# Optimization experiments

Measured on AMD Instinct MI355X. Metric: run time of the kernel, lower is better.

## Reference

```python
import jax, jax.numpy as jnp
import numpy as np

N_NODES = 50000
N_EDGES = 800000
IN_CH = 128
HID_CH = 128
OUT_CH = 10
NUM_GRAPHS = 128


def setup_inputs() -> dict:
    key = jax.random.key(0)
    ks = jax.random.split(key, 10)
    x = jax.random.normal(ks[0], (N_NODES, IN_CH), dtype=jnp.float32)
    edge_index = jax.random.randint(ks[1], (2, N_EDGES), 0, N_NODES, dtype=jnp.int64)
    batch = jnp.sort(jax.random.randint(ks[2], (N_NODES,), 0, NUM_GRAPHS, dtype=jnp.int64))
    s1 = 1.0 / np.sqrt(IN_CH)
    s2 = 1.0 / np.sqrt(HID_CH)
    W1 = jax.random.uniform(ks[3], (IN_CH, HID_CH), jnp.float32, -s1, s1)
    b1 = jnp.zeros((HID_CH,), jnp.float32)
    W2 = jax.random.uniform(ks[4], (HID_CH, HID_CH), jnp.float32, -s2, s2)
    b2 = jnp.zeros((HID_CH,), jnp.float32)
    Wc = jax.random.uniform(ks[5], (HID_CH, OUT_CH), jnp.float32, -s2, s2)
    bc = jax.random.uniform(ks[6], (OUT_CH,), jnp.float32, -s2, s2)
    return {"x": x, "edge_index": edge_index, "batch": batch,
            "W1": W1, "b1": b1, "W2": W2, "b2": b2, "Wc": Wc, "bc": bc}


def _gcn_norm(edge_index, num_nodes):
    # add self-loops, compute symmetric normalization deg^-1/2[src]*deg^-1/2[dst]
    loop = jnp.arange(num_nodes, dtype=edge_index.dtype)
    src = jnp.concatenate([edge_index[0], loop])
    dst = jnp.concatenate([edge_index[1], loop])
    deg = jax.ops.segment_sum(jnp.ones_like(dst, dtype=jnp.float32), dst,
                              num_segments=num_nodes)
    dinv = jnp.where(deg > 0, jax.lax.rsqrt(deg), 0.0)
    norm = dinv[src] * dinv[dst]
    return src, dst, norm


def _gcn_conv(h, src, dst, norm, W, b, num_nodes):
    h = h @ W                                    # [N, out]
    msg = h[src] * norm[:, None]                 # [E+N, out] gather + scale
    agg = jax.ops.segment_sum(msg, dst, num_segments=num_nodes)
    return agg + b


def reference(x, edge_index, batch, W1, b1, W2, b2, Wc, bc):
    n = x.shape[0]
    src, dst, norm = _gcn_norm(edge_index, n)
    h = jax.nn.relu(_gcn_conv(x, src, dst, norm, W1, b1, n))
    h = jax.nn.relu(_gcn_conv(h, src, dst, norm, W2, b2, n))
    # global mean pool over graphs
    sums = jax.ops.segment_sum(h, batch, num_segments=NUM_GRAPHS)
    cnts = jax.ops.segment_sum(jnp.ones((n,), jnp.float32), batch,
                               num_segments=NUM_GRAPHS)
    pooled = sums / jnp.maximum(cnts, 1.0)[:, None]
    # dropout is identity in eval mode
    return pooled @ Wc + bc
```

## Files before the change

kernel.cpp:

```cpp
#include <hip/hip_runtime.h>

#define N_NODES 50000
#define N_EDGES 800000
#define CH 128
#define NOUT 10
#define NUM_GRAPHS 128
#define GR 64
#define GEMM_BLOCKS ((N_NODES + GR - 1) / GR)
#define FILL_SEGS 200
#define FILL_CHUNK (N_EDGES / FILL_SEGS)
#define DST_RANGE (N_NODES / 8)
#define DEG_CAP 64

typedef __attribute__((ext_vector_type(8))) short bf16x8;
typedef __attribute__((ext_vector_type(4))) float f32x4;

union FragU { uint4 u; bf16x8 s; };

__device__ __forceinline__ unsigned pack_bf16(float a, float b) {
    unsigned ua = __float_as_uint(a), ub = __float_as_uint(b);
    ua += 0x7fffu + ((ua >> 16) & 1u);
    ub += 0x7fffu + ((ub >> 16) & 1u);
    return (ua >> 16) | (ub & 0xffff0000u);
}

__device__ __forceinline__ unsigned short cvt_bf16(float v) {
    unsigned u = __float_as_uint(v);
    u += 0x7fffu + ((u >> 16) & 1u);
    return (unsigned short)(u >> 16);
}

__global__ __launch_bounds__(256) void k_prep(const float* __restrict__ W1,
                                              const float* __restrict__ W2,
                                              unsigned short* __restrict__ Wb1,
                                              unsigned short* __restrict__ Wb2,
                                              int* __restrict__ fill_pos,
                                              float* __restrict__ psum) {
    if (blockIdx.x < 2) {
        const float* W = blockIdx.x ? W2 : W1;
        unsigned short* Wb = blockIdx.x ? Wb2 : Wb1;
        for (int i = threadIdx.x; i < CH * CH; i += 256) {
            int k = i >> 7, n = i & 127;
            Wb[((((k >> 3) << 7) + n) << 3) + (k & 7)] = cvt_bf16(W[i]);
        }
    } else if (blockIdx.x < 198) {
        int idx = (blockIdx.x - 2) * 256 + threadIdx.x;
        if (idx < N_NODES) fill_pos[idx] = 0;
    } else {
        psum[(blockIdx.x - 198) * 256 + threadIdx.x] = 0.f;
    }
}

template <bool SCALE>
__device__ __forceinline__ void gemm_body9(const float* __restrict__ X,
                                           const unsigned short* __restrict__ Wb,
                                           unsigned short* __restrict__ Yb,
                                           const int* __restrict__ cnt,
                                           int bid) {
    const int tid = threadIdx.x;
    const int w = tid >> 6;
    const int lane = tid & 63;
    const int m = lane & 15;
    const int quad = lane >> 4;
    const int row0 = bid * GR + w * 16;

    int row_a = row0 + m;
    if (row_a > N_NODES - 1) row_a = N_NODES - 1;
    const float4* Xr = (const float4*)(X + (size_t)row_a * CH) + quad * 2;

    float4 a[8];
    #pragma unroll
    for (int ks = 0; ks < 4; ++ks) {
        a[ks * 2]     = Xr[ks * 8];
        a[ks * 2 + 1] = Xr[ks * 8 + 1];
    }

    f32x4 acc[8];
    #pragma unroll
    for (int ct = 0; ct < 8; ++ct) acc[ct] = (f32x4){0.f, 0.f, 0.f, 0.f};

    const uint4* Wq = (const uint4*)Wb;
    #pragma unroll
    for (int ks = 0; ks < 4; ++ks) {
        FragU af;
        af.u.x = pack_bf16(a[ks * 2].x, a[ks * 2].y);
        af.u.y = pack_bf16(a[ks * 2].z, a[ks * 2].w);
        af.u.z = pack_bf16(a[ks * 2 + 1].x, a[ks * 2 + 1].y);
        af.u.w = pack_bf16(a[ks * 2 + 1].z, a[ks * 2 + 1].w);
        const int kg = ks * 4 + quad;
        #pragma unroll
        for (int ct = 0; ct < 8; ++ct) {
            FragU bfu;
            bfu.u = Wq[kg * 128 + ct * 16 + m];
            acc[ct] = __builtin_amdgcn_mfma_f32_16x16x32_bf16(af.s, bfu.s, acc[ct], 0, 0, 0);
        }
    }

    #pragma unroll
    for (int r = 0; r < 4; ++r) {
        int row = row0 + quad * 4 + r;
        if (row < N_NODES) {
            float dv = SCALE ? rsqrtf((float)(cnt[row] + 1)) : 1.0f;
            unsigned short* yrow = Yb + (size_t)row * CH + m;
            #pragma unroll
            for (int ct = 0; ct < 8; ++ct)
                yrow[ct * 16] = cvt_bf16(SCALE ? acc[ct][r] * dv : acc[ct][r]);
        }
    }
}

__global__ __launch_bounds__(256) void k_gemm_fill(const float* __restrict__ X,
                                                   const unsigned short* __restrict__ Wb,
                                                   unsigned short* __restrict__ Yb,
                                                   const int* __restrict__ src,
                                                   const int* __restrict__ dst,
                                                   int* __restrict__ fill_pos,
                                                   int* __restrict__ csr_src) {
    if (blockIdx.x < GEMM_BLOCKS) {
        gemm_body9<false>(X, Wb, Yb, nullptr, blockIdx.x);
    } else {
        const int b = blockIdx.x - GEMM_BLOCKS;
        const int rng = b & 7;
        const int seg = b >> 3;
        const int lo = rng * DST_RANGE, hi = lo + DST_RANGE;
        const int base = seg * FILL_CHUNK;
        for (int it = threadIdx.x * 4; it < FILL_CHUNK; it += 1024) {
            int e = base + it;
            int4 d4 = *(const int4*)(dst + e);
            #pragma unroll
            for (int k = 0; k < 4; ++k) {
                int d = (&d4.x)[k];
                if (d >= lo && d < hi) {
                    int slot = atomicAdd(&fill_pos[d], 1);
                    if (slot < DEG_CAP) csr_src[(d << 6) + slot] = src[e + k];
                }
            }
        }
    }
}

__global__ __launch_bounds__(256) void k_gemm9b(const float* __restrict__ X,
                                                const unsigned short* __restrict__ Wb,
                                                unsigned short* __restrict__ Yb,
                                                const int* __restrict__ cnt) {
    gemm_body9<true>(X, Wb, Yb, cnt, blockIdx.x);
}

template <bool HAS_W, bool POOL>
__device__ __forceinline__ void gather_body(const unsigned* __restrict__ tb,
                                            const int* __restrict__ csr_src,
                                            const int* __restrict__ cnt,
                                            const float* __restrict__ bias,
                                            float* __restrict__ h,
                                            const int* __restrict__ batch,
                                            float* __restrict__ psum) {
    const int wid = threadIdx.x >> 6;
    const int lane = threadIdx.x & 63;
    const int sub = lane >> 4;
    const int cidx = lane & 15;
    const int v = blockIdx.x * 4 + wid;

    int lenc = cnt[v];
    const float dv = rsqrtf((float)(lenc + 1));
    int len = lenc > DEG_CAP ? DEG_CAP : lenc;

    int u_l = 0;
    float w_l = 0.f;
    if (lane < len) {
        u_l = csr_src[(v << 6) + lane];
        if (HAS_W) w_l = rsqrtf((float)(cnt[u_l] + 1));
    }

    const uint4* tbq = (const uint4*)tb;
    float x[8];
    #pragma unroll
    for (int t = 0; t < 8; ++t) x[t] = 0.f;

    int j = 0;
    for (; j + 8 <= len; j += 8) {
        int i0 = j + sub, i1 = j + 4 + sub;
        int ua = __shfl(u_l, i0);
        int ub = __shfl(u_l, i1);
        float wa = HAS_W ? __shfl(w_l, i0) : 1.f;
        float wb = HAS_W ? __shfl(w_l, i1) : 1.f;
        uint4 qa = tbq[(size_t)ua * 16 + cidx];
        uint4 qb = tbq[(size_t)ub * 16 + cidx];
        #pragma unroll
        for (int t = 0; t < 4; ++t) {
            unsigned ra = ((const unsigned*)&qa)[t];
            x[2 * t]     = fmaf(wa, __uint_as_float(ra << 16), x[2 * t]);
            x[2 * t + 1] = fmaf(wa, __uint_as_float(ra & 0xffff0000u), x[2 * t + 1]);
        }
        #pragma unroll
        for (int t = 0; t < 4; ++t) {
            unsigned rb = ((const unsigned*)&qb)[t];
            x[2 * t]     = fmaf(wb, __uint_as_float(rb << 16), x[2 * t]);
            x[2 * t + 1] = fmaf(wb, __uint_as_float(rb & 0xffff0000u), x[2 * t + 1]);
        }
    }
    for (; j < len; j += 4) {
        int idx = j + sub;
        bool act = idx < len;
        int idx_c = act ? idx : 0;
        int u = __shfl(u_l, idx_c);
        float w;
        if (HAS_W) { float ws = __shfl(w_l, idx_c); w = act ? ws : 0.f; }
        else       { w = act ? 1.f : 0.f; }
        uint4 q = tbq[(size_t)u * 16 + cidx];
        #pragma unroll
        for (int t = 0; t < 4; ++t) {
            unsigned r = ((const unsigned*)&q)[t];
            x[2 * t]     = fmaf(w, __uint_as_float(r << 16), x[2 * t]);
            x[2 * t + 1] = fmaf(w, __uint_as_float(r & 0xffff0000u), x[2 * t + 1]);
        }
    }
    {
        uint4 q = tbq[(size_t)v * 16 + cidx];
        float w = (sub == 0) ? (HAS_W ? dv : 1.f) : 0.f;
        #pragma unroll
        for (int t = 0; t < 4; ++t) {
            unsigned r = ((const unsigned*)&q)[t];
            x[2 * t]     = fmaf(w, __uint_as_float(r << 16), x[2 * t]);
            x[2 * t + 1] = fmaf(w, __uint_as_float(r & 0xffff0000u), x[2 * t + 1]);
        }
    }

    #pragma unroll
    for (int t = 0; t < 8; ++t) {
        x[t] += __shfl_xor(x[t], 16);
        x[t] += __shfl_xor(x[t], 32);
    }

    const float4* b4 = (const float4*)bias;
    float4 b0 = b4[cidx * 2], b1 = b4[cidx * 2 + 1];
    float4 o0, o1;
    o0.x = fmaxf(fmaf(dv, x[0], b0.x), 0.f);
    o0.y = fmaxf(fmaf(dv, x[1], b0.y), 0.f);
    o0.z = fmaxf(fmaf(dv, x[2], b0.z), 0.f);
    o0.w = fmaxf(fmaf(dv, x[3], b0.w), 0.f);
    o1.x = fmaxf(fmaf(dv, x[4], b1.x), 0.f);
    o1.y = fmaxf(fmaf(dv, x[5], b1.y), 0.f);
    o1.z = fmaxf(fmaf(dv, x[6], b1.z), 0.f);
    o1.w = fmaxf(fmaf(dv, x[7], b1.w), 0.f);

    if (POOL) {
        __shared__ float sh[4][128];
        __shared__ int sg[4];
        if (lane == 0) sg[wid] = batch[v];
        if (sub == 0) {
            *(float4*)&sh[wid][cidx * 8]     = o0;
            *(float4*)&sh[wid][cidx * 8 + 4] = o1;
        }
        __syncthreads();
        const int tid = threadIdx.x;
        if (tid < 128) {
            int g0 = sg[0], g1 = sg[1], g2 = sg[2], g3 = sg[3];
            float v0 = sh[0][tid], v1 = sh[1][tid], v2 = sh[2][tid], v3 = sh[3][tid];
            if (g0 == g3) {
                atomicAdd(&psum[g0 * CH + tid], v0 + v1 + v2 + v3);
            } else {
                if (g0 == g1) v1 += v0; else atomicAdd(&psum[g0 * CH + tid], v0);
                if (g1 == g2) v2 += v1; else atomicAdd(&psum[g1 * CH + tid], v1);
                if (g2 == g3) v3 += v2; else atomicAdd(&psum[g2 * CH + tid], v2);
                atomicAdd(&psum[g3 * CH + tid], v3);
            }
        }
    } else {
        if (sub == 0) {
            float4* hq = (float4*)(h + (size_t)v * CH);
            hq[cidx * 2]     = o0;
            hq[cidx * 2 + 1] = o1;
        }
    }
}

__global__ __launch_bounds__(256) void k_gather_hw(const unsigned* __restrict__ tb,
                                                   const int* __restrict__ csr_src,
                                                   const int* __restrict__ cnt,
                                                   const float* __restrict__ b,
                                                   float* __restrict__ h) {
    gather_body<true, false>(tb, csr_src, cnt, b, h, nullptr, nullptr);
}

__global__ __launch_bounds__(256) void k_gather_pool(const unsigned* __restrict__ tb,
                                                     const int* __restrict__ csr_src,
                                                     const int* __restrict__ cnt,
                                                     const float* __restrict__ b,
                                                     const int* __restrict__ batch,
                                                     float* __restrict__ psum) {
    gather_body<false, true>(tb, csr_src, cnt, b, nullptr, batch, psum);
}

__global__ __launch_bounds__(128) void k_classify(const float* __restrict__ psum,
                                                  const int* __restrict__ batch,
                                                  const float* __restrict__ Wc,
                                                  const float* __restrict__ bc,
                                                  float* __restrict__ out) {
    __shared__ float p[CH];
    __shared__ float sinv;
    int g = blockIdx.x;
    int tid = threadIdx.x;
    if (tid == 0) {
        int lo = 0, hi = N_NODES;
        while (lo < hi) { int mid = (lo + hi) >> 1; if (batch[mid] < g) lo = mid + 1; else hi = mid; }
        int start = lo;
        lo = 0; hi = N_NODES;
        while (lo < hi) { int mid = (lo + hi) >> 1; if (batch[mid] < g + 1) lo = mid + 1; else hi = mid; }
        sinv = 1.0f / fmaxf((float)(lo - start), 1.0f);
    }
    __syncthreads();
    p[tid] = psum[g * CH + tid] * sinv;
    __syncthreads();
    if (tid < NOUT) {
        float acc = bc[tid];
        #pragma unroll 4
        for (int k = 0; k < CH; ++k) acc += p[k] * Wc[k * NOUT + tid];
        out[g * NOUT + tid] = acc;
    }
}

extern "C" void kernel_launch(void* const* d_in, const int* in_sizes, int n_in,
                              void* d_out, int out_size, void* d_ws, size_t ws_size,
                              hipStream_t stream) {
    const float* x     = (const float*)d_in[0];
    const int*   ei    = (const int*)d_in[1];
    const int*   batch = (const int*)d_in[2];
    const float* W1    = (const float*)d_in[3];
    const float* b1    = (const float*)d_in[4];
    const float* W2    = (const float*)d_in[5];
    const float* b2    = (const float*)d_in[6];
    const float* Wc    = (const float*)d_in[7];
    const float* bc    = (const float*)d_in[8];
    float* out = (float*)d_out;

    const int* src = ei;
    const int* dst = ei + N_EDGES;

    int*            fill_pos = (int*)d_ws;
    int*            csr_src  = fill_pos + N_NODES;
    unsigned short* wb1      = (unsigned short*)(csr_src + (size_t)N_NODES * DEG_CAP);
    unsigned short* wb2      = wb1 + CH * CH;
    unsigned short* tb       = wb2 + CH * CH;
    float*          hbuf     = (float*)(tb + (size_t)N_NODES * CH);
    float*          psum     = hbuf + (size_t)N_NODES * CH;

    k_prep<<<198 + 64, 256, 0, stream>>>(W1, W2, wb1, wb2, fill_pos, psum);

    k_gemm_fill<<<GEMM_BLOCKS + FILL_SEGS * 8, 256, 0, stream>>>(
        x, wb1, tb, src, dst, fill_pos, csr_src);

    k_gather_hw<<<N_NODES / 4, 256, 0, stream>>>((unsigned*)tb, csr_src, fill_pos, b1, hbuf);

    k_gemm9b<<<GEMM_BLOCKS, 256, 0, stream>>>(hbuf, wb2, tb, fill_pos);

    k_gather_pool<<<N_NODES / 4, 256, 0, stream>>>((unsigned*)tb, csr_src, fill_pos, b2,
                                                   batch, psum);

    k_classify<<<NUM_GRAPHS, 128, 0, stream>>>(psum, batch, Wc, bc, out);
}
```

Baseline: 246.5 us.

## Store hidden layer in bf16, vectorize GEMM output stores, unroll gather loop

The first gather now writes the hidden activations as packed bf16 instead of fp32. The second GEMM loads these bf16 A-fragments directly, with no fp32 load-and-convert step. The GEMM B-fragment indexing is permuted so each lane owns 8 contiguous output columns, which lets the output be written as a single 16-byte store instead of eight scalar 2-byte stores. The CSR fill loads src as an int4 vector, its blocks are ordered before the GEMM blocks, and the gather loop is restructured to issue up to four row loads before accumulating. The aim is less memory traffic and more loads in flight, at the cost of extra bf16 rounding on the intermediate activations.

```diff
diff --git a/kernel.cpp b/kernel.cpp
--- a/kernel.cpp
+++ b/kernel.cpp
@@ -9,6 +9,7 @@
 #define GEMM_BLOCKS ((N_NODES + GR - 1) / GR)
 #define FILL_SEGS 200
 #define FILL_CHUNK (N_EDGES / FILL_SEGS)
+#define FILL_BLOCKS (FILL_SEGS * 8)
 #define DST_RANGE (N_NODES / 8)
 #define DEG_CAP 64
 
@@ -51,8 +52,8 @@
     }
 }
 
-template <bool SCALE>
-__device__ __forceinline__ void gemm_body9(const float* __restrict__ X,
+template <bool SCALE, bool ABF16>
+__device__ __forceinline__ void gemm_body9(const void* __restrict__ X,
                                            const unsigned short* __restrict__ Wb,
                                            unsigned short* __restrict__ Yb,
                                            const int* __restrict__ cnt,
@@ -66,33 +67,42 @@
 
     int row_a = row0 + m;
     if (row_a > N_NODES - 1) row_a = N_NODES - 1;
-    const float4* Xr = (const float4*)(X + (size_t)row_a * CH) + quad * 2;
-
-    float4 a[8];
+
+    FragU af[4];
+    if (ABF16) {
+        const uint4* Xr = (const uint4*)((const unsigned short*)X + (size_t)row_a * CH);
+        #pragma unroll
+        for (int ks = 0; ks < 4; ++ks) af[ks].u = Xr[ks * 4 + quad];
+    } else {
+        const float4* Xr = (const float4*)((const float*)X + (size_t)row_a * CH) + quad * 2;
+        float4 a[8];
+        #pragma unroll
+        for (int ks = 0; ks < 4; ++ks) {
+            a[ks * 2]     = Xr[ks * 8];
+            a[ks * 2 + 1] = Xr[ks * 8 + 1];
+        }
+        #pragma unroll
+        for (int ks = 0; ks < 4; ++ks) {
+            af[ks].u.x = pack_bf16(a[ks * 2].x, a[ks * 2].y);
+            af[ks].u.y = pack_bf16(a[ks * 2].z, a[ks * 2].w);
+            af[ks].u.z = pack_bf16(a[ks * 2 + 1].x, a[ks * 2 + 1].y);
+            af[ks].u.w = pack_bf16(a[ks * 2 + 1].z, a[ks * 2 + 1].w);
+        }
+    }
+
+    f32x4 acc[8];
+    #pragma unroll
+    for (int ct = 0; ct < 8; ++ct) acc[ct] = (f32x4){0.f, 0.f, 0.f, 0.f};
+
+    const uint4* Wq = (const uint4*)Wb;
     #pragma unroll
     for (int ks = 0; ks < 4; ++ks) {
-        a[ks * 2]     = Xr[ks * 8];
-        a[ks * 2 + 1] = Xr[ks * 8 + 1];
-    }
-
-    f32x4 acc[8];
-    #pragma unroll
-    for (int ct = 0; ct < 8; ++ct) acc[ct] = (f32x4){0.f, 0.f, 0.f, 0.f};
-
-    const uint4* Wq = (const uint4*)Wb;
-    #pragma unroll
-    for (int ks = 0; ks < 4; ++ks) {
-        FragU af;
-        af.u.x = pack_bf16(a[ks * 2].x, a[ks * 2].y);
-        af.u.y = pack_bf16(a[ks * 2].z, a[ks * 2].w);
-        af.u.z = pack_bf16(a[ks * 2 + 1].x, a[ks * 2 + 1].y);
-        af.u.w = pack_bf16(a[ks * 2 + 1].z, a[ks * 2 + 1].w);
         const int kg = ks * 4 + quad;
         #pragma unroll
         for (int ct = 0; ct < 8; ++ct) {
             FragU bfu;
-            bfu.u = Wq[kg * 128 + ct * 16 + m];
-            acc[ct] = __builtin_amdgcn_mfma_f32_16x16x32_bf16(af.s, bfu.s, acc[ct], 0, 0, 0);
+            bfu.u = Wq[kg * 128 + m * 8 + ct];
+            acc[ct] = __builtin_amdgcn_mfma_f32_16x16x32_bf16(af[ks].s, bfu.s, acc[ct], 0, 0, 0);
         }
     }
 
@@ -100,11 +110,13 @@
     for (int r = 0; r < 4; ++r) {
         int row = row0 + quad * 4 + r;
         if (row < N_NODES) {
-            float dv = SCALE ? rsqrtf((float)(cnt[row] + 1)) : 1.0f;
-            unsigned short* yrow = Yb + (size_t)row * CH + m;
-            #pragma unroll
-            for (int ct = 0; ct < 8; ++ct)
-                yrow[ct * 16] = cvt_bf16(SCALE ? acc[ct][r] * dv : acc[ct][r]);
+            float s = SCALE ? rsqrtf((float)(cnt[row] + 1)) : 1.0f;
+            uint4 o;
+            o.x = pack_bf16(acc[0][r] * s, acc[1][r] * s);
+            o.y = pack_bf16(acc[2][r] * s, acc[3][r] * s);
+            o.z = pack_bf16(acc[4][r] * s, acc[5][r] * s);
+            o.w = pack_bf16(acc[6][r] * s, acc[7][r] * s);
+            *(uint4*)(Yb + (size_t)row * CH + m * 8) = o;
         }
     }
 }
@@ -116,10 +128,8 @@
                                                    const int* __restrict__ dst,
                                                    int* __restrict__ fill_pos,
                                                    int* __restrict__ csr_src) {
-    if (blockIdx.x < GEMM_BLOCKS) {
-        gemm_body9<false>(X, Wb, Yb, nullptr, blockIdx.x);
-    } else {
-        const int b = blockIdx.x - GEMM_BLOCKS;
+    if (blockIdx.x < FILL_BLOCKS) {
+        const int b = blockIdx.x;
         const int rng = b & 7;
         const int seg = b >> 3;
         const int lo = rng * DST_RANGE, hi = lo + DST_RANGE;
@@ -127,23 +137,35 @@
         for (int it = threadIdx.x * 4; it < FILL_CHUNK; it += 1024) {
             int e = base + it;
             int4 d4 = *(const int4*)(dst + e);
+            int4 s4 = *(const int4*)(src + e);
             #pragma unroll
             for (int k = 0; k < 4; ++k) {
                 int d = (&d4.x)[k];
                 if (d >= lo && d < hi) {
                     int slot = atomicAdd(&fill_pos[d], 1);
-                    if (slot < DEG_CAP) csr_src[(d << 6) + slot] = src[e + k];
+                    if (slot < DEG_CAP) csr_src[(d << 6) + slot] = (&s4.x)[k];
                 }
             }
         }
-    }
-}
-
-__global__ __launch_bounds__(256) void k_gemm9b(const float* __restrict__ X,
+    } else {
+        gemm_body9<false, false>(X, Wb, Yb, nullptr, blockIdx.x - FILL_BLOCKS);
+    }
+}
+
+__global__ __launch_bounds__(256) void k_gemm9b(const unsigned short* __restrict__ Xb,
                                                 const unsigned short* __restrict__ Wb,
                                                 unsigned short* __restrict__ Yb,
                                                 const int* __restrict__ cnt) {
-    gemm_body9<true>(X, Wb, Yb, cnt, blockIdx.x);
+    gemm_body9<true, true>(Xb, Wb, Yb, cnt, blockIdx.x);
+}
+
+__device__ __forceinline__ void acc_row(float (&x)[8], uint4 q, float w) {
+    #pragma unroll
+    for (int t = 0; t < 4; ++t) {
+        unsigned r = ((const unsigned*)&q)[t];
+        x[2 * t]     = fmaf(w, __uint_as_float(r << 16), x[2 * t]);
+        x[2 * t + 1] = fmaf(w, __uint_as_float(r & 0xffff0000u), x[2 * t + 1]);
+    }
 }
 
 template <bool HAS_W, bool POOL>
@@ -151,7 +173,7 @@
                                             const int* __restrict__ csr_src,
                                             const int* __restrict__ cnt,
                                             const float* __restrict__ bias,
-                                            float* __restrict__ h,
+                                            unsigned short* __restrict__ hb,
                                             const int* __restrict__ batch,
                                             float* __restrict__ psum) {
     const int wid = threadIdx.x >> 6;
@@ -176,53 +198,44 @@
     #pragma unroll
     for (int t = 0; t < 8; ++t) x[t] = 0.f;
 
-    int j = 0;
-    for (; j + 8 <= len; j += 8) {
-        int i0 = j + sub, i1 = j + 4 + sub;
-        int ua = __shfl(u_l, i0);
-        int ub = __shfl(u_l, i1);
-        float wa = HAS_W ? __shfl(w_l, i0) : 1.f;
-        float wb = HAS_W ? __shfl(w_l, i1) : 1.f;
-        uint4 qa = tbq[(size_t)ua * 16 + cidx];
-        uint4 qb = tbq[(size_t)ub * 16 + cidx];
-        #pragma unroll
-        for (int t = 0; t < 4; ++t) {
-            unsigned ra = ((const unsigned*)&qa)[t];
-            x[2 * t]     = fmaf(wa, __uint_as_float(ra << 16), x[2 * t]);
-            x[2 * t + 1] = fmaf(wa, __uint_as_float(ra & 0xffff0000u), x[2 * t + 1]);
-        }
-        #pragma unroll
-        for (int t = 0; t < 4; ++t) {
-            unsigned rb = ((const unsigned*)&qb)[t];
-            x[2 * t]     = fmaf(wb, __uint_as_float(rb << 16), x[2 * t]);
-            x[2 * t + 1] = fmaf(wb, __uint_as_float(rb & 0xffff0000u), x[2 * t + 1]);
-        }
-    }
-    for (; j < len; j += 4) {
-        int idx = j + sub;
-        bool act = idx < len;
-        int idx_c = act ? idx : 0;
-        int u = __shfl(u_l, idx_c);
-        float w;
-        if (HAS_W) { float ws = __shfl(w_l, idx_c); w = act ? ws : 0.f; }
-        else       { w = act ? 1.f : 0.f; }
-        uint4 q = tbq[(size_t)u * 16 + cidx];
-        #pragma unroll
-        for (int t = 0; t < 4; ++t) {
-            unsigned r = ((const unsigned*)&q)[t];
-            x[2 * t]     = fmaf(w, __uint_as_float(r << 16), x[2 * t]);
-            x[2 * t + 1] = fmaf(w, __uint_as_float(r & 0xffff0000u), x[2 * t + 1]);
-        }
+    const int ng = (len + 3) >> 2;
+    for (int g = 0; g < ng; g += 4) {
+        uint4 q0, q1, q2, q3;
+        float w0, w1, w2, w3;
+        bool h1 = g + 1 < ng, h2 = g + 2 < ng, h3 = g + 3 < ng;
+        {
+            int idx = g * 4 + sub; bool act = idx < len; int ic = act ? idx : 0;
+            int u = __shfl(u_l, ic);
+            w0 = act ? (HAS_W ? __shfl(w_l, ic) : 1.f) : 0.f;
+            q0 = tbq[(size_t)u * 16 + cidx];
+        }
+        if (h1) {
+            int idx = (g + 1) * 4 + sub; bool act = idx < len; int ic = act ? idx : 0;
+            int u = __shfl(u_l, ic);
+            w1 = act ? (HAS_W ? __shfl(w_l, ic) : 1.f) : 0.f;
+            q1 = tbq[(size_t)u * 16 + cidx];
+        }
+        if (h2) {
+            int idx = (g + 2) * 4 + sub; bool act = idx < len; int ic = act ? idx : 0;
+            int u = __shfl(u_l, ic);
+            w2 = act ? (HAS_W ? __shfl(w_l, ic) : 1.f) : 0.f;
+            q2 = tbq[(size_t)u * 16 + cidx];
+        }
+        if (h3) {
+            int idx = (g + 3) * 4 + sub; bool act = idx < len; int ic = act ? idx : 0;
+            int u = __shfl(u_l, ic);
+            w3 = act ? (HAS_W ? __shfl(w_l, ic) : 1.f) : 0.f;
+            q3 = tbq[(size_t)u * 16 + cidx];
+        }
+        acc_row(x, q0, w0);
+        if (h1) acc_row(x, q1, w1);
+        if (h2) acc_row(x, q2, w2);
+        if (h3) acc_row(x, q3, w3);
     }
     {
         uint4 q = tbq[(size_t)v * 16 + cidx];
         float w = (sub == 0) ? (HAS_W ? dv : 1.f) : 0.f;
-        #pragma unroll
-        for (int t = 0; t < 4; ++t) {
-            unsigned r = ((const unsigned*)&q)[t];
-            x[2 * t]     = fmaf(w, __uint_as_float(r << 16), x[2 * t]);
-            x[2 * t + 1] = fmaf(w, __uint_as_float(r & 0xffff0000u), x[2 * t + 1]);
-        }
+        acc_row(x, q, w);
     }
 
     #pragma unroll
@@ -233,23 +246,24 @@
 
     const float4* b4 = (const float4*)bias;
     float4 b0 = b4[cidx * 2], b1 = b4[cidx * 2 + 1];
-    float4 o0, o1;
-    o0.x = fmaxf(fmaf(dv, x[0], b0.x), 0.f);
-    o0.y = fmaxf(fmaf(dv, x[1], b0.y), 0.f);
-    o0.z = fmaxf(fmaf(dv, x[2], b0.z), 0.f);
-    o0.w = fmaxf(fmaf(dv, x[3], b0.w), 0.f);
-    o1.x = fmaxf(fmaf(dv, x[4], b1.x), 0.f);
-    o1.y = fmaxf(fmaf(dv, x[5], b1.y), 0.f);
-    o1.z = fmaxf(fmaf(dv, x[6], b1.z), 0.f);
-    o1.w = fmaxf(fmaf(dv, x[7], b1.w), 0.f);
+    float o[8];
+    o[0] = fmaxf(fmaf(dv, x[0], b0.x), 0.f);
+    o[1] = fmaxf(fmaf(dv, x[1], b0.y), 0.f);
+    o[2] = fmaxf(fmaf(dv, x[2], b0.z), 0.f);
+    o[3] = fmaxf(fmaf(dv, x[3], b0.w), 0.f);
+    o[4] = fmaxf(fmaf(dv, x[4], b1.x), 0.f);
+    o[5] = fmaxf(fmaf(dv, x[5], b1.y), 0.f);
+    o[6] = fmaxf(fmaf(dv, x[6], b1.z), 0.f);
+    o[7] = fmaxf(fmaf(dv, x[7], b1.w), 0.f);
 
     if (POOL) {
         __shared__ float sh[4][128];
         __shared__ int sg[4];
         if (lane == 0) sg[wid] = batch[v];
         if (sub == 0) {
-            *(float4*)&sh[wid][cidx * 8]     = o0;
-            *(float4*)&sh[wid][cidx * 8 + 4] = o1;
+            float4* shp = (float4*)&sh[wid][cidx * 8];
+            shp[0] = (float4){o[0], o[1], o[2], o[3]};
+            shp[1] = (float4){o[4], o[5], o[6], o[7]};
         }
         __syncthreads();
         const int tid = threadIdx.x;
@@ -267,9 +281,12 @@
         }
     } else {
         if (sub == 0) {
-            float4* hq = (float4*)(h + (size_t)v * CH);
-            hq[cidx * 2]     = o0;
-            hq[cidx * 2 + 1] = o1;
+            uint4 ob;
+            ob.x = pack_bf16(o[0], o[1]);
+            ob.y = pack_bf16(o[2], o[3]);
+            ob.z = pack_bf16(o[4], o[5]);
+            ob.w = pack_bf16(o[6], o[7]);
+            *(uint4*)(hb + (size_t)v * CH + cidx * 8) = ob;
         }
     }
 }
@@ -278,8 +295,8 @@
                                                    const int* __restrict__ csr_src,
                                                    const int* __restrict__ cnt,
                                                    const float* __restrict__ b,
-                                                   float* __restrict__ h) {
-    gather_body<true, false>(tb, csr_src, cnt, b, h, nullptr, nullptr);
+                                                   unsigned short* __restrict__ hb) {
+    gather_body<true, false>(tb, csr_src, cnt, b, hb, nullptr, nullptr);
 }
 
 __global__ __launch_bounds__(256) void k_gather_pool(const unsigned* __restrict__ tb,
@@ -341,17 +358,17 @@
     unsigned short* wb1      = (unsigned short*)(csr_src + (size_t)N_NODES * DEG_CAP);
     unsigned short* wb2      = wb1 + CH * CH;
     unsigned short* tb       = wb2 + CH * CH;
-    float*          hbuf     = (float*)(tb + (size_t)N_NODES * CH);
-    float*          psum     = hbuf + (size_t)N_NODES * CH;
+    unsigned short* hb16     = tb + (size_t)N_NODES * CH;
+    float*          psum     = (float*)(hb16 + (size_t)N_NODES * CH);
 
     k_prep<<<198 + 64, 256, 0, stream>>>(W1, W2, wb1, wb2, fill_pos, psum);
 
-    k_gemm_fill<<<GEMM_BLOCKS + FILL_SEGS * 8, 256, 0, stream>>>(
+    k_gemm_fill<<<FILL_BLOCKS + GEMM_BLOCKS, 256, 0, stream>>>(
         x, wb1, tb, src, dst, fill_pos, csr_src);
 
-    k_gather_hw<<<N_NODES / 4, 256, 0, stream>>>((unsigned*)tb, csr_src, fill_pos, b1, hbuf);
-
-    k_gemm9b<<<GEMM_BLOCKS, 256, 0, stream>>>(hbuf, wb2, tb, fill_pos);
+    k_gather_hw<<<N_NODES / 4, 256, 0, stream>>>((unsigned*)tb, csr_src, fill_pos, b1, hb16);
+
+    k_gemm9b<<<GEMM_BLOCKS, 256, 0, stream>>>(hb16, wb2, tb, fill_pos);
 
     k_gather_pool<<<N_NODES / 4, 256, 0, stream>>>((unsigned*)tb, csr_src, fill_pos, b2,
                                                    batch, psum);
```

New measurement: 260.7 us. +5.7%, slower.

## Replace range-partitioned CSR fill with single-pass edge-chunked fill

Applied to the files above, without the earlier changes.

The CSR fill no longer has each edge segment scanned by 8 blocks, each of which keeps only destinations in its own node range. Each block now handles a 2048-edge chunk once, reading dst and src with vector int4 loads and issuing atomics for every edge. This removes the 8x redundant reads of dst and the scalar src loads. In exchange it loses the locality of the atomics and scattered writes within a node range, which may raise cache contention on fill_pos and csr_src.

```diff
diff --git a/kernel.cpp b/kernel.cpp
--- a/kernel.cpp
+++ b/kernel.cpp
@@ -7,9 +7,8 @@
 #define NUM_GRAPHS 128
 #define GR 64
 #define GEMM_BLOCKS ((N_NODES + GR - 1) / GR)
-#define FILL_SEGS 200
-#define FILL_CHUNK (N_EDGES / FILL_SEGS)
-#define DST_RANGE (N_NODES / 8)
+#define FILL_EPB 2048
+#define FILL_BLOCKS ((N_EDGES + FILL_EPB - 1) / FILL_EPB)
 #define DEG_CAP 64
 
 typedef __attribute__((ext_vector_type(8))) short bf16x8;
@@ -120,19 +119,25 @@
         gemm_body9<false>(X, Wb, Yb, nullptr, blockIdx.x);
     } else {
         const int b = blockIdx.x - GEMM_BLOCKS;
-        const int rng = b & 7;
-        const int seg = b >> 3;
-        const int lo = rng * DST_RANGE, hi = lo + DST_RANGE;
-        const int base = seg * FILL_CHUNK;
-        for (int it = threadIdx.x * 4; it < FILL_CHUNK; it += 1024) {
-            int e = base + it;
-            int4 d4 = *(const int4*)(dst + e);
-            #pragma unroll
-            for (int k = 0; k < 4; ++k) {
-                int d = (&d4.x)[k];
-                if (d >= lo && d < hi) {
+        const int base = b * FILL_EPB;
+        int4 d4[2], s4[2];
+        #pragma unroll
+        for (int i = 0; i < 2; ++i) {
+            int e = base + ((int)threadIdx.x + i * 256) * 4;
+            if (e < N_EDGES) {
+                d4[i] = *(const int4*)(dst + e);
+                s4[i] = *(const int4*)(src + e);
+            }
+        }
+        #pragma unroll
+        for (int i = 0; i < 2; ++i) {
+            int e = base + ((int)threadIdx.x + i * 256) * 4;
+            if (e < N_EDGES) {
+                #pragma unroll
+                for (int k = 0; k < 4; ++k) {
+                    int d = (&d4[i].x)[k];
                     int slot = atomicAdd(&fill_pos[d], 1);
-                    if (slot < DEG_CAP) csr_src[(d << 6) + slot] = src[e + k];
+                    if (slot < DEG_CAP) csr_src[(d << 6) + slot] = (&s4[i].x)[k];
                 }
             }
         }
@@ -346,7 +351,7 @@
 
     k_prep<<<198 + 64, 256, 0, stream>>>(W1, W2, wb1, wb2, fill_pos, psum);
 
-    k_gemm_fill<<<GEMM_BLOCKS + FILL_SEGS * 8, 256, 0, stream>>>(
+    k_gemm_fill<<<GEMM_BLOCKS + FILL_BLOCKS, 256, 0, stream>>>(
         x, wb1, tb, src, dst, fill_pos, csr_src);
 
     k_gather_hw<<<N_NODES / 4, 256, 0, stream>>>((unsigned*)tb, csr_src, fill_pos, b1, hbuf);
```

Result: slower. 257.0 us (+4.2%).

## Split gather kernels by channel half and prefetch all neighbor rows upfront

Applied to the files above, without the earlier changes.

Each node's 128-channel aggregation is now split across two blocks, one per 64-channel half. Each wave processes 8 neighbor rows at once (8 lanes per row) instead of 4. All neighbor-row loads, up to 8 per lane, are issued before any accumulation, to raise memory-level parallelism in the latency-bound gather. In exchange there are twice as many blocks, cnt and csr_src are read twice per node, there are more shuffle reductions, and extra registers are held for the prefetched rows.

```diff
diff --git a/kernel.cpp b/kernel.cpp
--- a/kernel.cpp
+++ b/kernel.cpp
@@ -5,12 +5,14 @@
 #define CH 128
 #define NOUT 10
 #define NUM_GRAPHS 128
+#define POOL_CHUNK 50
 #define GR 64
 #define GEMM_BLOCKS ((N_NODES + GR - 1) / GR)
 #define FILL_SEGS 200
 #define FILL_CHUNK (N_EDGES / FILL_SEGS)
 #define DST_RANGE (N_NODES / 8)
 #define DEG_CAP 64
+#define GATHER_BLOCKS (N_NODES / 4 * 2)
 
 typedef __attribute__((ext_vector_type(8))) short bf16x8;
 typedef __attribute__((ext_vector_type(4))) float f32x4;
@@ -146,19 +148,32 @@
     gemm_body9<true>(X, Wb, Yb, cnt, blockIdx.x);
 }
 
+__device__ __forceinline__ void acc_row(float (&x)[8], uint4 q, float w) {
+    #pragma unroll
+    for (int t = 0; t < 4; ++t) {
+        unsigned r = ((const unsigned*)&q)[t];
+        x[2 * t]     = fmaf(w, __uint_as_float(r << 16), x[2 * t]);
+        x[2 * t + 1] = fmaf(w, __uint_as_float(r & 0xffff0000u), x[2 * t + 1]);
+    }
+}
+
 template <bool HAS_W, bool POOL>
-__device__ __forceinline__ void gather_body(const unsigned* __restrict__ tb,
-                                            const int* __restrict__ csr_src,
-                                            const int* __restrict__ cnt,
-                                            const float* __restrict__ bias,
-                                            float* __restrict__ h,
-                                            const int* __restrict__ batch,
-                                            float* __restrict__ psum) {
-    const int wid = threadIdx.x >> 6;
-    const int lane = threadIdx.x & 63;
-    const int sub = lane >> 4;
-    const int cidx = lane & 15;
-    const int v = blockIdx.x * 4 + wid;
+__device__ __forceinline__ void gather_half_body(const uint4* __restrict__ tbq,
+                                                 const int* __restrict__ csr_src,
+                                                 const int* __restrict__ cnt,
+                                                 const float* __restrict__ bias,
+                                                 float* __restrict__ h,
+                                                 const int* __restrict__ batch,
+                                                 float* __restrict__ psum) {
+    const int tid = threadIdx.x;
+    const int wid = tid >> 6;
+    const int lane = tid & 63;
+    const int sub = lane >> 3;
+    const int cidx = lane & 7;
+    const int r = blockIdx.x & 7;
+    const int half = r >> 2;
+    const int vg = (blockIdx.x >> 3) * 4 + (r & 3);
+    const int v = vg * 4 + wid;
 
     int lenc = cnt[v];
     const float dv = rsqrtf((float)(lenc + 1));
@@ -171,105 +186,78 @@
         if (HAS_W) w_l = rsqrtf((float)(cnt[u_l] + 1));
     }
 
-    const uint4* tbq = (const uint4*)tb;
+    const int nb = (len + 7) >> 3;
+    uint4 q[8];
+    float w[8];
+    #pragma unroll
+    for (int k = 0; k < 8; ++k) {
+        if (k < nb) {
+            int ridx = k * 8 + sub;
+            bool act = ridx < len;
+            int ic = act ? ridx : 0;
+            int u = __shfl(u_l, ic);
+            float ws = HAS_W ? __shfl(w_l, ic) : 1.f;
+            w[k] = act ? ws : 0.f;
+            q[k] = tbq[(size_t)u * 16 + half * 8 + cidx];
+        }
+    }
+    uint4 qs = tbq[(size_t)v * 16 + half * 8 + cidx];
+
     float x[8];
     #pragma unroll
     for (int t = 0; t < 8; ++t) x[t] = 0.f;
-
-    int j = 0;
-    for (; j + 8 <= len; j += 8) {
-        int i0 = j + sub, i1 = j + 4 + sub;
-        int ua = __shfl(u_l, i0);
-        int ub = __shfl(u_l, i1);
-        float wa = HAS_W ? __shfl(w_l, i0) : 1.f;
-        float wb = HAS_W ? __shfl(w_l, i1) : 1.f;
-        uint4 qa = tbq[(size_t)ua * 16 + cidx];
-        uint4 qb = tbq[(size_t)ub * 16 + cidx];
-        #pragma unroll
-        for (int t = 0; t < 4; ++t) {
-            unsigned ra = ((const unsigned*)&qa)[t];
-            x[2 * t]     = fmaf(wa, __uint_as_float(ra << 16), x[2 * t]);
-            x[2 * t + 1] = fmaf(wa, __uint_as_float(ra & 0xffff0000u), x[2 * t + 1]);
-        }
-        #pragma unroll
-        for (int t = 0; t < 4; ++t) {
-            unsigned rb = ((const unsigned*)&qb)[t];
-            x[2 * t]     = fmaf(wb, __uint_as_float(rb << 16), x[2 * t]);
-            x[2 * t + 1] = fmaf(wb, __uint_as_float(rb & 0xffff0000u), x[2 * t + 1]);
-        }
-    }
-    for (; j < len; j += 4) {
-        int idx = j + sub;
-        bool act = idx < len;
-        int idx_c = act ? idx : 0;
-        int u = __shfl(u_l, idx_c);
-        float w;
-        if (HAS_W) { float ws = __shfl(w_l, idx_c); w = act ? ws : 0.f; }
-        else       { w = act ? 1.f : 0.f; }
-        uint4 q = tbq[(size_t)u * 16 + cidx];
-        #pragma unroll
-        for (int t = 0; t < 4; ++t) {
-            unsigned r = ((const unsigned*)&q)[t];
-            x[2 * t]     = fmaf(w, __uint_as_float(r << 16), x[2 * t]);
-            x[2 * t + 1] = fmaf(w, __uint_as_float(r & 0xffff0000u), x[2 * t + 1]);
-        }
-    }
-    {
-        uint4 q = tbq[(size_t)v * 16 + cidx];
-        float w = (sub == 0) ? (HAS_W ? dv : 1.f) : 0.f;
-        #pragma unroll
-        for (int t = 0; t < 4; ++t) {
-            unsigned r = ((const unsigned*)&q)[t];
-            x[2 * t]     = fmaf(w, __uint_as_float(r << 16), x[2 * t]);
-            x[2 * t + 1] = fmaf(w, __uint_as_float(r & 0xffff0000u), x[2 * t + 1]);
-        }
-    }
+    #pragma unroll
+    for (int k = 0; k < 8; ++k)
+        if (k < nb) acc_row(x, q[k], w[k]);
+    acc_row(x, qs, (sub == 0) ? (HAS_W ? dv : 1.f) : 0.f);
 
     #pragma unroll
     for (int t = 0; t < 8; ++t) {
+        x[t] += __shfl_xor(x[t], 8);
         x[t] += __shfl_xor(x[t], 16);
         x[t] += __shfl_xor(x[t], 32);
     }
 
     const float4* b4 = (const float4*)bias;
-    float4 b0 = b4[cidx * 2], b1 = b4[cidx * 2 + 1];
-    float4 o0, o1;
-    o0.x = fmaxf(fmaf(dv, x[0], b0.x), 0.f);
-    o0.y = fmaxf(fmaf(dv, x[1], b0.y), 0.f);
-    o0.z = fmaxf(fmaf(dv, x[2], b0.z), 0.f);
-    o0.w = fmaxf(fmaf(dv, x[3], b0.w), 0.f);
-    o1.x = fmaxf(fmaf(dv, x[4], b1.x), 0.f);
-    o1.y = fmaxf(fmaf(dv, x[5], b1.y), 0.f);
-    o1.z = fmaxf(fmaf(dv, x[6], b1.z), 0.f);
-    o1.w = fmaxf(fmaf(dv, x[7], b1.w), 0.f);
+    float4 b0 = b4[half * 16 + cidx * 2], b1v = b4[half * 16 + cidx * 2 + 1];
+    float o[8];
+    o[0] = fmaxf(fmaf(dv, x[0], b0.x), 0.f);
+    o[1] = fmaxf(fmaf(dv, x[1], b0.y), 0.f);
+    o[2] = fmaxf(fmaf(dv, x[2], b0.z), 0.f);
+    o[3] = fmaxf(fmaf(dv, x[3], b0.w), 0.f);
+    o[4] = fmaxf(fmaf(dv, x[4], b1v.x), 0.f);
+    o[5] = fmaxf(fmaf(dv, x[5], b1v.y), 0.f);
+    o[6] = fmaxf(fmaf(dv, x[6], b1v.z), 0.f);
+    o[7] = fmaxf(fmaf(dv, x[7], b1v.w), 0.f);
 
     if (POOL) {
-        __shared__ float sh[4][128];
+        __shared__ float sh[4][64];
         __shared__ int sg[4];
         if (lane == 0) sg[wid] = batch[v];
         if (sub == 0) {
-            *(float4*)&sh[wid][cidx * 8]     = o0;
-            *(float4*)&sh[wid][cidx * 8 + 4] = o1;
+            float4* shp = (float4*)&sh[wid][cidx * 8];
+            shp[0] = (float4){o[0], o[1], o[2], o[3]};
+            shp[1] = (float4){o[4], o[5], o[6], o[7]};
         }
         __syncthreads();
-        const int tid = threadIdx.x;
-        if (tid < 128) {
+        if (tid < 64) {
+            const int ch = half * 64 + tid;
             int g0 = sg[0], g1 = sg[1], g2 = sg[2], g3 = sg[3];
             float v0 = sh[0][tid], v1 = sh[1][tid], v2 = sh[2][tid], v3 = sh[3][tid];
             if (g0 == g3) {
-                atomicAdd(&psum[g0 * CH + tid], v0 + v1 + v2 + v3);
+                atomicAdd(&psum[g0 * CH + ch], v0 + v1 + v2 + v3);
             } else {
-                if (g0 == g1) v1 += v0; else atomicAdd(&psum[g0 * CH + tid], v0);
-                if (g1 == g2) v2 += v1; else atomicAdd(&psum[g1 * CH + tid], v1);
-                if (g2 == g3) v3 += v2; else atomicAdd(&psum[g2 * CH + tid], v2);
-                atomicAdd(&psum[g3 * CH + tid], v3);
+                if (g0 == g1) v1 += v0; else atomicAdd(&psum[g0 * CH + ch], v0);
+                if (g1 == g2) v2 += v1; else atomicAdd(&psum[g1 * CH + ch], v1);
+                if (g2 == g3) v3 += v2; else atomicAdd(&psum[g2 * CH + ch], v2);
+                atomicAdd(&psum[g3 * CH + ch], v3);
             }
         }
     } else {
         if (sub == 0) {
-            float4* hq = (float4*)(h + (size_t)v * CH);
-            hq[cidx * 2]     = o0;
-            hq[cidx * 2 + 1] = o1;
+            float4* hq = (float4*)(h + (size_t)v * CH + half * 64 + cidx * 8);
+            hq[0] = (float4){o[0], o[1], o[2], o[3]};
+            hq[1] = (float4){o[4], o[5], o[6], o[7]};
         }
     }
 }
@@ -279,7 +267,7 @@
                                                    const int* __restrict__ cnt,
                                                    const float* __restrict__ b,
                                                    float* __restrict__ h) {
-    gather_body<true, false>(tb, csr_src, cnt, b, h, nullptr, nullptr);
+    gather_half_body<true, false>((const uint4*)tb, csr_src, cnt, b, h, nullptr, nullptr);
 }
 
 __global__ __launch_bounds__(256) void k_gather_pool(const unsigned* __restrict__ tb,
@@ -288,7 +276,7 @@
                                                      const float* __restrict__ b,
                                                      const int* __restrict__ batch,
                                                      float* __restrict__ psum) {
-    gather_body<false, true>(tb, csr_src, cnt, b, nullptr, batch, psum);
+    gather_half_body<false, true>((const uint4*)tb, csr_src, cnt, b, nullptr, batch, psum);
 }
 
 __global__ __launch_bounds__(128) void k_classify(const float* __restrict__ psum,
@@ -349,12 +337,13 @@
     k_gemm_fill<<<GEMM_BLOCKS + FILL_SEGS * 8, 256, 0, stream>>>(
         x, wb1, tb, src, dst, fill_pos, csr_src);
 
-    k_gather_hw<<<N_NODES / 4, 256, 0, stream>>>((unsigned*)tb, csr_src, fill_pos, b1, hbuf);
+    k_gather_hw<<<GATHER_BLOCKS, 256, 0, stream>>>((unsigned*)tb, csr_src, fill_pos,
+                                                   b1, hbuf);
 
     k_gemm9b<<<GEMM_BLOCKS, 256, 0, stream>>>(hbuf, wb2, tb, fill_pos);
 
-    k_gather_pool<<<N_NODES / 4, 256, 0, stream>>>((unsigned*)tb, csr_src, fill_pos, b2,
-                                                   batch, psum);
+    k_gather_pool<<<GATHER_BLOCKS, 256, 0, stream>>>((unsigned*)tb, csr_src, fill_pos,
+                                                     b2, batch, psum);
 
     k_classify<<<NUM_GRAPHS, 128, 0, stream>>>(psum, batch, Wc, bc, out);
 }
```

Result: slower. 277.4 us (+12.5%).
